# Kernel optimization log

Measured on AMD Instinct MI355X. Metric: run time of the kernel, lower is better.

The kernel has to match this reference:

```python
import jax, jax.numpy as jnp
import numpy as np
from jax import lax

DN = ('NCHW', 'OIHW', 'NCHW')


def conv3x3(x, w, b):
    return lax.conv_general_dilated(x, w, (1, 1), 'SAME', dimension_numbers=DN) + b[None, :, None, None]


def conv1x1(x, w, b):
    # w: [O, I] -> pointwise conv
    return jnp.einsum('oi,bihw->bohw', w, x) + b[None, :, None, None]


def sft(x0, x1, sc0w, sc0b, sc1w, sc1b, sh0w, sh0b, sh1w, sh1b):
    scale = conv1x1(jax.nn.leaky_relu(conv1x1(x1, sc0w, sc0b), 0.1), sc1w, sc1b)
    shift = conv1x1(jax.nn.leaky_relu(conv1x1(x1, sh0w, sh0b), 0.1), sh1w, sh1b)
    return x0 * (scale + 1.0) + shift


def deform_conv(x, offset, w, b):
    # torchvision DeformConv2d, 3x3, stride 1, pad 1, dilation 1, no mask.
    B, C, H, W = x.shape
    O = w.shape[0]
    K = 9
    off = offset.reshape(B, K, 2, H, W)  # (dy, dx) per kernel tap
    ki = jnp.arange(3, dtype=x.dtype) - 1.0
    ky = jnp.repeat(ki, 3)  # [9]
    kx = jnp.tile(ki, 3)
    hh = jnp.arange(H, dtype=x.dtype)
    ww = jnp.arange(W, dtype=x.dtype)
    py = off[:, :, 0] + hh[None, None, :, None] + ky[None, :, None, None]  # [B,K,H,W]
    px = off[:, :, 1] + ww[None, None, None, :] + kx[None, :, None, None]
    y0f = jnp.floor(py)
    x0f = jnp.floor(px)
    wy = (py - y0f)[:, None]  # [B,1,K,H,W]
    wx = (px - x0f)[:, None]
    y0 = y0f.astype(jnp.int32)
    x0i = x0f.astype(jnp.int32)
    x_flat = x.reshape(B, C, H * W)

    def gather(iy, ix):
        valid = (iy >= 0) & (iy < H) & (ix >= 0) & (ix < W)
        idx = (jnp.clip(iy, 0, H - 1) * W + jnp.clip(ix, 0, W - 1)).reshape(B, K * H * W)
        vals = jax.vmap(lambda xf, ii: xf[:, ii])(x_flat, idx)  # [B,C,K*H*W]
        return vals.reshape(B, C, K, H, W) * valid[:, None].astype(x.dtype)

    v00 = gather(y0, x0i)
    v01 = gather(y0, x0i + 1)
    v10 = gather(y0 + 1, x0i)
    v11 = gather(y0 + 1, x0i + 1)
    samp = (v00 * (1 - wy) * (1 - wx) + v01 * (1 - wy) * wx
            + v10 * wy * (1 - wx) + v11 * wy * wx)  # [B,C,K,H,W]
    return jnp.einsum('bckhw,ock->bohw', samp, w.reshape(O, C, K)) + b[None, :, None, None]


def setup_inputs() -> dict:
    key = jax.random.key(0)
    ks = jax.random.split(key, 32)
    B, C0, C1, H, W = 4, 128, 32, 96, 96
    f32 = jnp.float32
    d = {
        'x0': jax.random.normal(ks[0], (B, C0, H, W), f32),
        'x1': jax.random.normal(ks[1], (B, C1, H, W), f32),
        'w_off': jax.random.normal(ks[2], (18, C0, 3, 3), f32) * 0.02,
        'b_off': jnp.zeros((18,), f32),
        's1_sc0_w': jax.random.normal(ks[3], (C0, C1), f32) * 0.05,
        's1_sc0_b': jnp.zeros((C0,), f32),
        's1_sc1_w': jax.random.normal(ks[4], (C0, C0), f32) * 0.05,
        's1_sc1_b': jnp.zeros((C0,), f32),
        's1_sh0_w': jax.random.normal(ks[5], (C0, C1), f32) * 0.05,
        's1_sh0_b': jnp.zeros((C0,), f32),
        's1_sh1_w': jax.random.normal(ks[6], (C0, C0), f32) * 0.05,
        's1_sh1_b': jnp.zeros((C0,), f32),
        'w_d1': jax.random.normal(ks[7], (C0, C0, 3, 3), f32) * 0.03,
        'b_d1': jnp.zeros((C0,), f32),
        's2_sc0_w': jax.random.normal(ks[8], (C0, C1), f32) * 0.05,
        's2_sc0_b': jnp.zeros((C0,), f32),
        's2_sc1_w': jax.random.normal(ks[9], (C0, C0), f32) * 0.05,
        's2_sc1_b': jnp.zeros((C0,), f32),
        's2_sh0_w': jax.random.normal(ks[10], (C0, C1), f32) * 0.05,
        's2_sh0_b': jnp.zeros((C0,), f32),
        's2_sh1_w': jax.random.normal(ks[11], (C0, C0), f32) * 0.05,
        's2_sh1_b': jnp.zeros((C0,), f32),
        'w_d2': jax.random.normal(ks[12], (C0, C0, 3, 3), f32) * 0.03,
        'b_d2': jnp.zeros((C0,), f32),
    }
    return d


def reference(x0, x1, w_off, b_off,
              s1_sc0_w, s1_sc0_b, s1_sc1_w, s1_sc1_b,
              s1_sh0_w, s1_sh0_b, s1_sh1_w, s1_sh1_b,
              w_d1, b_d1,
              s2_sc0_w, s2_sc0_b, s2_sc1_w, s2_sc1_b,
              s2_sh0_w, s2_sh0_b, s2_sh1_w, s2_sh1_b,
              w_d2, b_d2):
    off = conv3x3(x0, w_off, b_off)
    fea = sft(x0, x1, s1_sc0_w, s1_sc0_b, s1_sc1_w, s1_sc1_b,
              s1_sh0_w, s1_sh0_b, s1_sh1_w, s1_sh1_b)
    fea = jax.nn.relu(deform_conv(fea, off, w_d1, b_d1))
    fea = sft(fea, x1, s2_sc0_w, s2_sc0_b, s2_sc1_w, s2_sc1_b,
              s2_sh0_w, s2_sh0_b, s2_sh1_w, s2_sh1_b)
    fea = deform_conv(fea, off, w_d2, b_d2)
    return x0 + fea
```

## Files before the change

### kernel.cpp

```cpp
#include <hip/hip_runtime.h>

typedef unsigned short u16;
typedef unsigned int   u32;
typedef __attribute__((ext_vector_type(8))) _Float16 f16x8;
typedef __attribute__((ext_vector_type(2))) float f32x2;
typedef __attribute__((ext_vector_type(4))) float f32x4;
typedef __attribute__((ext_vector_type(4))) unsigned int u32x4;

constexpr int B_  = 4;
constexpr int C0  = 128;
constexpr int C1  = 32;
constexpr int H_  = 96;
constexpr int W_  = 96;
constexpr int HW  = H_ * W_;
constexpr int PT  = 64;
constexpr int TPB = HW / PT;
constexpr int NTILE = B_ * TPB;

__device__ inline u16 f2h(float f) {
    _Float16 h = (_Float16)f;
    return __builtin_bit_cast(u16, h);
}

__global__ __launch_bounds__(256) void k_prep(
    const float* __restrict__ w_off,
    const float* __restrict__ wd1,  const float* __restrict__ wd2,
    const float* __restrict__ s1c0, const float* __restrict__ s1h0,
    const float* __restrict__ s2c0, const float* __restrict__ s2h0,
    const float* __restrict__ s1c1, const float* __restrict__ s1h1,
    const float* __restrict__ s2c1, const float* __restrict__ s2h1,
    float* __restrict__ wofft, u16* __restrict__ wdhi, u16* __restrict__ wdlo,
    u16* __restrict__ w0h,     u16* __restrict__ w1h)
{
    int t = blockIdx.x * 256 + threadIdx.x;
    if (t < C0 * 18 * 9) {
        int c = t / 162, r = t % 162, o = r / 9, tap = r % 9;
        wofft[t] = w_off[(o * C0 + c) * 9 + tap];
    }
    if (t < 2 * 9 * C0 * C0) {
        int d = t / (9 * C0 * C0), r = t % (9 * C0 * C0);
        int k = r / (C0 * C0), r2 = r % (C0 * C0), o = r2 / C0, c = r2 % C0;
        const float* wsrc = d ? wd2 : wd1;
        float wv = wsrc[(o * C0 + c) * 9 + k];
        _Float16 hi = (_Float16)wv;
        float rr = wv - (float)hi;
        wdhi[t] = __builtin_bit_cast(u16, hi);
        wdlo[t] = f2h(rr);
    }
    if (t < 4 * C0 * C1) {
        int m = t / (C0 * C1), i = t % (C0 * C1);
        const float* s = (m == 0) ? s1c0 : (m == 1) ? s1h0 : (m == 2) ? s2c0 : s2h0;
        w0h[t] = f2h(s[i]);
    }
    if (t < 4 * C0 * C0) {
        int m = t / (C0 * C0), i = t % (C0 * C0);
        const float* s = (m == 0) ? s1c1 : (m == 1) ? s1h1 : (m == 2) ? s2c1 : s2h1;
        w1h[t] = f2h(s[i]);
    }
}

__global__ __launch_bounds__(256) void k_conv_off(
    const float* __restrict__ x0, const float* __restrict__ wofft,
    const float* __restrict__ boff, float* __restrict__ off)
{
    int bx = blockIdx.x;
    int b  = bx / TPB;
    int p0 = (bx % TPB) * PT;
    int tid = threadIdx.x;
    int p   = tid & 63;
    int cq  = __builtin_amdgcn_readfirstlane(tid >> 6);
    int pos = p0 + p;
    int h = pos / W_, w = pos % W_;

    float acc[18];
#pragma unroll
    for (int o = 0; o < 18; ++o) acc[o] = 0.f;

    for (int cc = 0; cc < 32; ++cc) {
        int c = cq * 32 + cc;
        const float* xb = x0 + ((size_t)(b * C0 + c)) * HW;
        float v[9];
#pragma unroll
        for (int t = 0; t < 9; ++t) {
            int dy = t / 3 - 1, dx = t % 3 - 1;
            int hy = h + dy, wx = w + dx;
            bool ok = (hy >= 0) & (hy < H_) & (wx >= 0) & (wx < W_);
            v[t] = ok ? xb[hy * W_ + wx] : 0.f;
        }
        const float* wr = wofft + c * 162;
#pragma unroll
        for (int o = 0; o < 18; ++o)
#pragma unroll
            for (int t = 0; t < 9; ++t)
                acc[o] = fmaf(wr[o * 9 + t], v[t], acc[o]);
    }

    __shared__ float red[4][18][PT];
#pragma unroll
    for (int o = 0; o < 18; ++o) red[cq][o][p] = acc[o];
    __syncthreads();
    for (int idx = tid; idx < 18 * PT; idx += 256) {
        int o = idx / PT, pp = idx % PT;
        float s = red[0][o][pp] + red[1][o][pp] + red[2][o][pp] + red[3][o][pp]
                + boff[o];
        off[((size_t)(b * 18 + o)) * HW + p0 + pp] = s;
    }
}

template <int XSRC>
__global__ __launch_bounds__(512) void k_sft_mma(
    const float* __restrict__ xf,
    const float* __restrict__ xT,
    const float* __restrict__ x1,
    const u16* __restrict__ w0s, const u16* __restrict__ w0h,
    const u16* __restrict__ w1s, const u16* __restrict__ w1h,
    const float* __restrict__ b0s, const float* __restrict__ b0h,
    const float* __restrict__ b1s, const float* __restrict__ b1h,
    float* __restrict__ outT)
{
    __shared__ __align__(16) u16   x1t[64 * 32];
    __shared__ __align__(16) u16   hidt[2][64 * 128];
    __shared__ __align__(16) float outt[64 * 128];

    int bx = blockIdx.x, b = bx / TPB, p0 = (bx % TPB) * PT;
    int tid = threadIdx.x, l = tid & 63;
    int w = __builtin_amdgcn_readfirstlane(tid >> 6);
    f32x4 zz = {0.f, 0.f, 0.f, 0.f};

    for (int i = tid; i < C1 * PT; i += 512) {
        int ch = i >> 6, pos = i & 63;
        float v = x1[((size_t)(b * C1 + ch)) * HW + p0 + pos];
        x1t[pos * 32 + (ch ^ ((pos & 3) << 3))] = f2h(v);
    }
    __syncthreads();

    {
        int mt = w & 3, br = w >> 2;
        int pos = mt * 16 + (l & 15);
        int koff = (l >> 4) * 8;
        f16x8 a = *(const f16x8*)&x1t[pos * 32 + (koff ^ ((pos & 3) << 3))];
        const u16* w0 = br ? w0h : w0s;
        const float* bb = br ? b0h : b0s;
        u16* hrow = hidt[br];
#pragma unroll
        for (int nt = 0; nt < 8; ++nt) {
            int n = nt * 16 + (l & 15);
            f16x8 bfr = *(const f16x8*)&w0[n * 32 + koff];
            f32x4 h = __builtin_amdgcn_mfma_f32_16x16x32_f16(a, bfr, zz, 0, 0, 0);
            float bv = bb[n];
#pragma unroll
            for (int r = 0; r < 4; ++r) {
                float hv = h[r] + bv;
                hv = hv > 0.f ? hv : 0.1f * hv;
                int prow = mt * 16 + (l >> 4) * 4 + r;
                hrow[prow * 128 + (n ^ ((prow & 7) << 3))] = f2h(hv);
            }
        }
    }
    __syncthreads();

    f32x4 accS[4], accH[4];
#pragma unroll
    for (int nt = 0; nt < 4; ++nt) { accS[nt] = zz; accH[nt] = zz; }
    int mt = w & 3, nh = w >> 2;
    int pos = mt * 16 + (l & 15);
#pragma unroll
    for (int ks = 0; ks < 4; ++ks) {
        int kb = ks * 32 + (l >> 4) * 8;
        f16x8 aS = *(const f16x8*)&hidt[0][pos * 128 + (kb ^ ((pos & 7) << 3))];
        f16x8 aH = *(const f16x8*)&hidt[1][pos * 128 + (kb ^ ((pos & 7) << 3))];
#pragma unroll
        for (int nt = 0; nt < 4; ++nt) {
            int n = nh * 64 + nt * 16 + (l & 15);
            f16x8 bS = *(const f16x8*)&w1s[n * 128 + kb];
            f16x8 bH = *(const f16x8*)&w1h[n * 128 + kb];
            accS[nt] = __builtin_amdgcn_mfma_f32_16x16x32_f16(aS, bS, accS[nt], 0, 0, 0);
            accH[nt] = __builtin_amdgcn_mfma_f32_16x16x32_f16(aH, bH, accH[nt], 0, 0, 0);
        }
    }

#pragma unroll
    for (int nt = 0; nt < 4; ++nt) {
        int n = nh * 64 + nt * 16 + (l & 15);
        float scb = b1s[n], shb = b1h[n];
        float xv[4];
        if (XSRC == 0) {
            const float* xp = xf + ((size_t)(b * C0 + n)) * HW + p0 + mt * 16 + (l >> 4) * 4;
            f32x4 x4 = *(const f32x4*)xp;
#pragma unroll
            for (int r = 0; r < 4; ++r) xv[r] = x4[r];
        } else {
#pragma unroll
            for (int r = 0; r < 4; ++r)
                xv[r] = xT[((size_t)(b * HW + p0 + mt * 16 + (l >> 4) * 4 + r)) * C0 + n];
        }
#pragma unroll
        for (int r = 0; r < 4; ++r) {
            float scale = accS[nt][r] + scb + 1.f;
            float shift = accH[nt][r] + shb;
            outt[(mt * 16 + (l >> 4) * 4 + r) * 128 + n] = xv[r] * scale + shift;
        }
    }
    __syncthreads();

    float* dst = outT + ((size_t)(b * HW + p0)) * C0;
    for (int i = tid; i < 2048; i += 512)
        *(f32x4*)&dst[i * 4] = *(const f32x4*)&outt[i * 4];
}

template <int MODE>
__global__ __launch_bounds__(512, 4) void k_deform5(
    const float* __restrict__ srcT,
    const float* __restrict__ off,
    const u16* __restrict__ whi,
    const u16* __restrict__ wlo,
    const float* __restrict__ bias,
    const float* __restrict__ x0,
    float* __restrict__ outF,
    float* __restrict__ outT)
{
    constexpr int S = 136;
    __shared__ __align__(16) u16   smem[4 * 64 * S];
    __shared__ __align__(16) u16   cidx[9 * 64 * 4];
    __shared__ __align__(16) float cwt[9 * 64 * 2];
    u16* a_hi = smem;
    u16* a_lo = smem + 64 * S;
    u16* b_hi = smem + 2 * 64 * S;
    u16* b_lo = smem + 3 * 64 * S;

    int bx = blockIdx.x;
    bx = (bx & 7) * (NTILE / 8) + (bx >> 3);
    int b = bx / TPB, p0 = (bx % TPB) * PT;
    int tid = threadIdx.x, l = tid & 63;
    int w = __builtin_amdgcn_readfirstlane(tid >> 6);
    f32x4 zz = {0.f, 0.f, 0.f, 0.f};

    for (int e = tid; e < 9 * 64; e += 512) {
        int k = e >> 6, pp = e & 63;
        int pos = p0 + pp, h = pos / W_, wc = pos % W_;
        float dy = off[((size_t)(b * 18 + 2 * k)) * HW + pos];
        float dx = off[((size_t)(b * 18 + 2 * k + 1)) * HW + pos];
        float py = dy + (float)(h + k / 3 - 1);
        float px = dx + (float)(wc + k % 3 - 1);
        float yf = floorf(py), xf = floorf(px);
        int y0 = (int)yf, x0i = (int)xf;
        cwt[e * 2]     = py - yf;
        cwt[e * 2 + 1] = px - xf;
        int iy0 = min(max(y0, 0), H_ - 1),     iy1 = min(max(y0 + 1, 0), H_ - 1);
        int ix0 = min(max(x0i, 0), W_ - 1),    ix1 = min(max(x0i + 1, 0), W_ - 1);
        bool vy0 = (y0 >= 0) & (y0 < H_),      vy1 = (y0 + 1 >= 0) & (y0 + 1 < H_);
        bool vx0 = (x0i >= 0) & (x0i < W_),    vx1 = (x0i + 1 >= 0) & (x0i + 1 < W_);
        cidx[e * 4 + 0] = (u16)(iy0 * W_ + ix0) | ((vy0 & vx0) ? 0x8000 : 0);
        cidx[e * 4 + 1] = (u16)(iy0 * W_ + ix1) | ((vy0 & vx1) ? 0x8000 : 0);
        cidx[e * 4 + 2] = (u16)(iy1 * W_ + ix0) | ((vy1 & vx0) ? 0x8000 : 0);
        cidx[e * 4 + 3] = (u16)(iy1 * W_ + ix1) | ((vy1 & vx1) ? 0x8000 : 0);
    }
    __syncthreads();

    f32x4 acc[2][2];
#pragma unroll
    for (int hf = 0; hf < 2; ++hf)
#pragma unroll
        for (int nt = 0; nt < 2; ++nt) acc[hf][nt] = zz;

    int mt = w & 3, ng = w >> 2;
    int pos_r = mt * 16 + (l & 15);
    int so = tid >> 3, sp = tid & 7;
    const float* base  = srcT + (size_t)b * HW * C0;
    const float* lbase = base + 2 * l;

    f32x2 gv1[4][4], gv2[4][4];
    u32x4 rbh0, rbh1, rbl0, rbl1;

#define ISSUE_A(DST, KK, IOFF)                                                \
    {                                                                         \
        int ek = (KK) * 64 + w * 8 + (IOFF);                                  \
        _Pragma("unroll")                                                     \
        for (int i = 0; i < 4; ++i) {                                         \
            int e = ek + i;                                                   \
            u32 c01 = *(const u32*)&cidx[e * 4];                              \
            u32 c23 = *(const u32*)&cidx[e * 4 + 2];                          \
            DST[i][0] = *(const f32x2*)(lbase + (size_t)(c01 & 0x3fffu) * C0);\
            DST[i][1] = *(const f32x2*)(lbase + (size_t)((c01 >> 16) & 0x3fffu) * C0); \
            DST[i][2] = *(const f32x2*)(lbase + (size_t)(c23 & 0x3fffu) * C0);\
            DST[i][3] = *(const f32x2*)(lbase + (size_t)((c23 >> 16) & 0x3fffu) * C0); \
        }                                                                     \
    }

#define COMMIT_HALF(SRC, KK, IOFF)                                            \
    {                                                                         \
        int ek = (KK) * 64 + w * 8 + (IOFF);                                  \
        _Pragma("unroll")                                                     \
        for (int i = 0; i < 4; ++i) {                                         \
            int e = ek + i, pp = w * 8 + (IOFF) + i;                          \
            u32 c01 = *(const u32*)&cidx[e * 4];                              \
            u32 c23 = *(const u32*)&cidx[e * 4 + 2];                          \
            float wy = cwt[e * 2], wx = cwt[e * 2 + 1];                       \
            float aa  = wy * wx;                                              \
            float w11 = (c23 & 0x80000000u) ? aa : 0.f;                       \
            float w10 = (c23 & 0x8000u) ? (wy - aa) : 0.f;                    \
            float w01 = (c01 & 0x80000000u) ? (wx - aa) : 0.f;                \
            float w00 = (c01 & 0x8000u) ? (1.f - wy - wx + aa) : 0.f;         \
            float s0 = SRC[i][0][0] * w00 + SRC[i][1][0] * w01                \
                     + SRC[i][2][0] * w10 + SRC[i][3][0] * w11;               \
            float s1 = SRC[i][0][1] * w00 + SRC[i][1][1] * w01                \
                     + SRC[i][2][1] * w10 + SRC[i][3][1] * w11;               \
            _Float16 h0 = (_Float16)s0, h1 = (_Float16)s1;                    \
            float r0 = s0 - (float)h0, r1 = s1 - (float)h1;                   \
            u32 hv = (u32)__builtin_bit_cast(u16, h0)                         \
                   | ((u32)__builtin_bit_cast(u16, h1) << 16);                \
            u32 lv = (u32)f2h(r0) | ((u32)f2h(r1) << 16);                     \
            *(u32*)&a_hi[pp * S + 2 * l] = hv;                                \
            *(u32*)&a_lo[pp * S + 2 * l] = lv;                                \
        }                                                                     \
    }

#define ISSUE_B(KK, HF)                                                       \
    {                                                                         \
        int orow = (HF) * 64 + so;                                            \
        const u16* sh = whi + ((size_t)(KK) * C0 + orow) * C0 + sp * 16;      \
        const u16* sl = wlo + ((size_t)(KK) * C0 + orow) * C0 + sp * 16;      \
        rbh0 = *(const u32x4*)&sh[0];  rbh1 = *(const u32x4*)&sh[8];          \
        rbl0 = *(const u32x4*)&sl[0];  rbl1 = *(const u32x4*)&sl[8];          \
    }

#define WRITE_B()                                                             \
    {                                                                         \
        *(u32x4*)&b_hi[so * S + sp * 16]     = rbh0;                          \
        *(u32x4*)&b_hi[so * S + sp * 16 + 8] = rbh1;                          \
        *(u32x4*)&b_lo[so * S + sp * 16]     = rbl0;                          \
        *(u32x4*)&b_lo[so * S + sp * 16 + 8] = rbl1;                          \
    }

#define MFMA_HALF(HF)                                                         \
    {                                                                         \
        _Pragma("unroll")                                                     \
        for (int ks = 0; ks < 4; ++ks) {                                      \
            int kb = ks * 32 + (l >> 4) * 8;                                  \
            int ai = pos_r * S + kb;                                          \
            f16x8 ah = *(const f16x8*)&a_hi[ai];                              \
            f16x8 al = *(const f16x8*)&a_lo[ai];                              \
            _Pragma("unroll")                                                 \
            for (int nt = 0; nt < 2; ++nt) {                                  \
                int orow = ng * 32 + nt * 16 + (l & 15);                      \
                int bi = orow * S + kb;                                       \
                f16x8 bh = *(const f16x8*)&b_hi[bi];                          \
                f16x8 bl = *(const f16x8*)&b_lo[bi];                          \
                acc[HF][nt] = __builtin_amdgcn_mfma_f32_16x16x32_f16(ah, bh, acc[HF][nt], 0, 0, 0); \
                acc[HF][nt] = __builtin_amdgcn_mfma_f32_16x16x32_f16(al, bh, acc[HF][nt], 0, 0, 0); \
                acc[HF][nt] = __builtin_amdgcn_mfma_f32_16x16x32_f16(ah, bl, acc[HF][nt], 0, 0, 0); \
            }                                                                 \
        }                                                                     \
    }

    ISSUE_A(gv1, 0, 0)
    ISSUE_A(gv2, 0, 4)
    ISSUE_B(0, 0)

    for (int k = 0; k < 9; ++k) {
        COMMIT_HALF(gv1, k, 0)
        COMMIT_HALF(gv2, k, 4)
        WRITE_B()
        ISSUE_B(k, 1)
        if (k < 8) ISSUE_A(gv1, k + 1, 0)
        __builtin_amdgcn_sched_barrier(0);
        __syncthreads();
        MFMA_HALF(0)
        __syncthreads();
        WRITE_B()
        if (k < 8) { ISSUE_B(k + 1, 0) }
        if (k < 8) { ISSUE_A(gv2, k + 1, 4) }
        __builtin_amdgcn_sched_barrier(0);
        __syncthreads();
        MFMA_HALF(1)
        __syncthreads();
    }
#undef ISSUE_A
#undef COMMIT_HALF
#undef ISSUE_B
#undef WRITE_B
#undef MFMA_HALF

    if (MODE == 0) {
        float* otile = (float*)smem;
#pragma unroll
        for (int hf = 0; hf < 2; ++hf)
#pragma unroll
            for (int nt = 0; nt < 2; ++nt) {
                int o = hf * 64 + ng * 32 + nt * 16 + (l & 15);
                float bv = bias[o];
#pragma unroll
                for (int r = 0; r < 4; ++r) {
                    float v = acc[hf][nt][r] + bv;
                    v = v > 0.f ? v : 0.f;
                    otile[(mt * 16 + (l >> 4) * 4 + r) * 132 + o] = v;
                }
            }
        __syncthreads();
        float* dst = outT + ((size_t)(b * HW + p0)) * C0;
        for (int i = tid; i < 2048; i += 512) {
            int row = i >> 5, c = i & 31;
            *(f32x4*)&dst[row * 128 + c * 4] = *(const f32x4*)&otile[row * 132 + c * 4];
        }
    } else {
#pragma unroll
        for (int hf = 0; hf < 2; ++hf)
#pragma unroll
            for (int nt = 0; nt < 2; ++nt) {
                int o = hf * 64 + ng * 32 + nt * 16 + (l & 15);
                float bv = bias[o];
                size_t base_o = ((size_t)(b * C0 + o)) * HW + p0 + mt * 16 + (l >> 4) * 4;
                f32x4 x4 = *(const f32x4*)(x0 + base_o);
                f32x4 ov;
#pragma unroll
                for (int r = 0; r < 4; ++r) ov[r] = acc[hf][nt][r] + bv + x4[r];
                *(f32x4*)(outF + base_o) = ov;
            }
    }
}

constexpr size_t WB_OFF   = 0;
constexpr size_t WB_WOFFT = 2654208;
constexpr size_t WB_W0H   = 2737152;
constexpr size_t WB_W1H   = 2769920;
constexpr size_t WB_WDHI  = 2900992;
constexpr size_t WB_WDLO  = 4080640;
constexpr size_t WB_TA    = 5260288;
constexpr size_t WB_TB    = 24134656;

extern "C" void kernel_launch(void* const* d_in, const int* in_sizes, int n_in,
                              void* d_out, int out_size, void* d_ws, size_t ws_size,
                              hipStream_t stream)
{
    const float* x0      = (const float*)d_in[0];
    const float* x1      = (const float*)d_in[1];
    const float* w_off   = (const float*)d_in[2];
    const float* b_off   = (const float*)d_in[3];
    const float* s1_sc0w = (const float*)d_in[4];
    const float* s1_sc0b = (const float*)d_in[5];
    const float* s1_sc1w = (const float*)d_in[6];
    const float* s1_sc1b = (const float*)d_in[7];
    const float* s1_sh0w = (const float*)d_in[8];
    const float* s1_sh0b = (const float*)d_in[9];
    const float* s1_sh1w = (const float*)d_in[10];
    const float* s1_sh1b = (const float*)d_in[11];
    const float* w_d1    = (const float*)d_in[12];
    const float* b_d1    = (const float*)d_in[13];
    const float* s2_sc0w = (const float*)d_in[14];
    const float* s2_sc0b = (const float*)d_in[15];
    const float* s2_sc1w = (const float*)d_in[16];
    const float* s2_sc1b = (const float*)d_in[17];
    const float* s2_sh0w = (const float*)d_in[18];
    const float* s2_sh0b = (const float*)d_in[19];
    const float* s2_sh1w = (const float*)d_in[20];
    const float* s2_sh1b = (const float*)d_in[21];
    const float* w_d2    = (const float*)d_in[22];
    const float* b_d2    = (const float*)d_in[23];

    char* wsb = (char*)d_ws;
    float* off   = (float*)(wsb + WB_OFF);
    float* wofft = (float*)(wsb + WB_WOFFT);
    u16*   w0h   = (u16*)(wsb + WB_W0H);
    u16*   w1h   = (u16*)(wsb + WB_W1H);
    u16*   wdhi  = (u16*)(wsb + WB_WDHI);
    u16*   wdlo  = (u16*)(wsb + WB_WDLO);
    float* TA    = (float*)(wsb + WB_TA);
    float* TB    = (float*)(wsb + WB_TB);

    k_prep<<<1152, 256, 0, stream>>>(w_off, w_d1, w_d2,
                                     s1_sc0w, s1_sh0w, s2_sc0w, s2_sh0w,
                                     s1_sc1w, s1_sh1w, s2_sc1w, s2_sh1w,
                                     wofft, wdhi, wdlo, w0h, w1h);
    k_conv_off<<<NTILE, 256, 0, stream>>>(x0, wofft, b_off, off);
    k_sft_mma<0><<<NTILE, 512, 0, stream>>>(x0, nullptr, x1,
                                            w0h, w0h + 4096,
                                            w1h, w1h + 16384,
                                            s1_sc0b, s1_sh0b, s1_sc1b, s1_sh1b, TA);
    k_deform5<0><<<NTILE, 512, 0, stream>>>(TA, off, wdhi, wdlo, b_d1,
                                            nullptr, nullptr, TB);
    k_sft_mma<1><<<NTILE, 512, 0, stream>>>(nullptr, TB, x1,
                                            w0h + 8192, w0h + 12288,
                                            w1h + 32768, w1h + 49152,
                                            s2_sc0b, s2_sh0b, s2_sc1b, s2_sh1b, TA);
    k_deform5<1><<<NTILE, 512, 0, stream>>>(TA, off, wdhi + 9 * 16384, wdlo + 9 * 16384,
                                            b_d2, x0, (float*)d_out, nullptr);
}
```

Baseline: 365.2 us.

## Restructure deform conv to 32x32 MFMA with K-halved weight staging

The deformable conv kernel now has each wave compute a 32x32 output tile with 32x32x16 f16 MFMAs instead of four 16x16 tiles. Weights are staged in 64-wide K halves, with full __syncthreads replaced by lgkmcnt waits plus s_barrier, and setprio raised around the MFMA phases. The SFT kernel drops its shared-memory output tile and writes its transposed output directly to global memory with a 6-block occupancy hint. The larger MFMA tile is meant to cut LDS traffic per flop. In exchange, the SFT stores become strided and less coalesced, and the lighter barrier scheme is harder to keep correct.

Measured after the change: 376.8 us. 1.03x slower.

```diff
diff --git a/kernel.cpp b/kernel.cpp
--- a/kernel.cpp
+++ b/kernel.cpp
@@ -5,6 +5,7 @@
 typedef __attribute__((ext_vector_type(8))) _Float16 f16x8;
 typedef __attribute__((ext_vector_type(2))) float f32x2;
 typedef __attribute__((ext_vector_type(4))) float f32x4;
+typedef __attribute__((ext_vector_type(16))) float f32x16;
 typedef __attribute__((ext_vector_type(4))) unsigned int u32x4;
 
 constexpr int B_  = 4;
@@ -108,7 +109,7 @@
 }
 
 template <int XSRC>
-__global__ __launch_bounds__(512) void k_sft_mma(
+__global__ __launch_bounds__(512, 6) void k_sft_mma(
     const float* __restrict__ xf,
     const float* __restrict__ xT,
     const float* __restrict__ x1,
@@ -118,9 +119,8 @@
     const float* __restrict__ b1s, const float* __restrict__ b1h,
     float* __restrict__ outT)
 {
-    __shared__ __align__(16) u16   x1t[64 * 32];
-    __shared__ __align__(16) u16   hidt[2][64 * 128];
-    __shared__ __align__(16) float outt[64 * 128];
+    __shared__ __align__(16) u16 x1t[64 * 32];
+    __shared__ __align__(16) u16 hidt[2][64 * 128];
 
     int bx = blockIdx.x, b = bx / TPB, p0 = (bx % TPB) * PT;
     int tid = threadIdx.x, l = tid & 63;
@@ -198,18 +198,14 @@
         for (int r = 0; r < 4; ++r) {
             float scale = accS[nt][r] + scb + 1.f;
             float shift = accH[nt][r] + shb;
-            outt[(mt * 16 + (l >> 4) * 4 + r) * 128 + n] = xv[r] * scale + shift;
-        }
-    }
-    __syncthreads();
-
-    float* dst = outT + ((size_t)(b * HW + p0)) * C0;
-    for (int i = tid; i < 2048; i += 512)
-        *(f32x4*)&dst[i * 4] = *(const f32x4*)&outt[i * 4];
+            outT[((size_t)(b * HW + p0 + mt * 16 + (l >> 4) * 4 + r)) * C0 + n]
+                = xv[r] * scale + shift;
+        }
+    }
 }
 
 template <int MODE>
-__global__ __launch_bounds__(512, 4) void k_deform5(
+__global__ __launch_bounds__(512, 4) void k_deform10(
     const float* __restrict__ srcT,
     const float* __restrict__ off,
     const u16* __restrict__ whi,
@@ -219,21 +215,20 @@
     float* __restrict__ outF,
     float* __restrict__ outT)
 {
-    constexpr int S = 136;
-    __shared__ __align__(16) u16   smem[4 * 64 * S];
+    constexpr int SA = 136;
+    constexpr int SB = 72;
+    __shared__ __align__(16) u16   a_buf[2][64 * SA];
+    __shared__ __align__(16) u16   b_buf[2][128 * SB];
     __shared__ __align__(16) u16   cidx[9 * 64 * 4];
     __shared__ __align__(16) float cwt[9 * 64 * 2];
-    u16* a_hi = smem;
-    u16* a_lo = smem + 64 * S;
-    u16* b_hi = smem + 2 * 64 * S;
-    u16* b_lo = smem + 3 * 64 * S;
 
     int bx = blockIdx.x;
     bx = (bx & 7) * (NTILE / 8) + (bx >> 3);
     int b = bx / TPB, p0 = (bx % TPB) * PT;
     int tid = threadIdx.x, l = tid & 63;
     int w = __builtin_amdgcn_readfirstlane(tid >> 6);
-    f32x4 zz = {0.f, 0.f, 0.f, 0.f};
+    int mh = w & 1, ng = w >> 1;
+    int lr = l & 31, ksel = l >> 5;
 
     for (int e = tid; e < 9 * 64; e += 512) {
         int k = e >> 6, pp = e & 63;
@@ -257,22 +252,17 @@
     }
     __syncthreads();
 
-    f32x4 acc[2][2];
-#pragma unroll
-    for (int hf = 0; hf < 2; ++hf)
-#pragma unroll
-        for (int nt = 0; nt < 2; ++nt) acc[hf][nt] = zz;
-
-    int mt = w & 3, ng = w >> 2;
-    int pos_r = mt * 16 + (l & 15);
-    int so = tid >> 3, sp = tid & 7;
-    const float* base  = srcT + (size_t)b * HW * C0;
-    const float* lbase = base + 2 * l;
+    f32x16 acc;
+#pragma unroll
+    for (int i = 0; i < 16; ++i) acc[i] = 0.f;
+
+    const float* lbase = srcT + (size_t)b * HW * C0 + 2 * l;
+    int wrow = tid >> 2, wseg = tid & 3;
 
     f32x2 gv1[4][4], gv2[4][4];
-    u32x4 rbh0, rbh1, rbl0, rbl1;
-
-#define ISSUE_A(DST, KK, IOFF)                                                \
+    u32x4 wbh[2], wbl[2];
+
+#define ISSUE_G(DST, KK, IOFF)                                                \
     {                                                                         \
         int ek = (KK) * 64 + w * 8 + (IOFF);                                  \
         _Pragma("unroll")                                                     \
@@ -287,7 +277,7 @@
         }                                                                     \
     }
 
-#define COMMIT_HALF(SRC, KK, IOFF)                                            \
+#define COMMIT_CH(SRC, KK, IOFF)                                              \
     {                                                                         \
         int ek = (KK) * 64 + w * 8 + (IOFF);                                  \
         _Pragma("unroll")                                                     \
@@ -310,92 +300,103 @@
             u32 hv = (u32)__builtin_bit_cast(u16, h0)                         \
                    | ((u32)__builtin_bit_cast(u16, h1) << 16);                \
             u32 lv = (u32)f2h(r0) | ((u32)f2h(r1) << 16);                     \
-            *(u32*)&a_hi[pp * S + 2 * l] = hv;                                \
-            *(u32*)&a_lo[pp * S + 2 * l] = lv;                                \
+            *(u32*)&a_buf[0][pp * SA + 2 * l] = hv;                           \
+            *(u32*)&a_buf[1][pp * SA + 2 * l] = lv;                           \
         }                                                                     \
     }
 
-#define ISSUE_B(KK, HF)                                                       \
+#define ISSUE_W(KK, KH)                                                       \
     {                                                                         \
-        int orow = (HF) * 64 + so;                                            \
-        const u16* sh = whi + ((size_t)(KK) * C0 + orow) * C0 + sp * 16;      \
-        const u16* sl = wlo + ((size_t)(KK) * C0 + orow) * C0 + sp * 16;      \
-        rbh0 = *(const u32x4*)&sh[0];  rbh1 = *(const u32x4*)&sh[8];          \
-        rbl0 = *(const u32x4*)&sl[0];  rbl1 = *(const u32x4*)&sl[8];          \
+        const u16* sh = whi + (size_t)(KK) * 16384 + wrow * 128 + (KH) * 64 + wseg * 16; \
+        const u16* sl = wlo + (size_t)(KK) * 16384 + wrow * 128 + (KH) * 64 + wseg * 16; \
+        wbh[0] = *(const u32x4*)&sh[0];  wbh[1] = *(const u32x4*)&sh[8];      \
+        wbl[0] = *(const u32x4*)&sl[0];  wbl[1] = *(const u32x4*)&sl[8];      \
     }
 
 #define WRITE_B()                                                             \
     {                                                                         \
-        *(u32x4*)&b_hi[so * S + sp * 16]     = rbh0;                          \
-        *(u32x4*)&b_hi[so * S + sp * 16 + 8] = rbh1;                          \
-        *(u32x4*)&b_lo[so * S + sp * 16]     = rbl0;                          \
-        *(u32x4*)&b_lo[so * S + sp * 16 + 8] = rbl1;                          \
-    }
-
-#define MFMA_HALF(HF)                                                         \
+        *(u32x4*)&b_buf[0][wrow * SB + wseg * 16]     = wbh[0];               \
+        *(u32x4*)&b_buf[0][wrow * SB + wseg * 16 + 8] = wbh[1];               \
+        *(u32x4*)&b_buf[1][wrow * SB + wseg * 16]     = wbl[0];               \
+        *(u32x4*)&b_buf[1][wrow * SB + wseg * 16 + 8] = wbl[1];               \
+    }
+
+#define MFMA_PH(KH)                                                           \
     {                                                                         \
         _Pragma("unroll")                                                     \
         for (int ks = 0; ks < 4; ++ks) {                                      \
-            int kb = ks * 32 + (l >> 4) * 8;                                  \
-            int ai = pos_r * S + kb;                                          \
-            f16x8 ah = *(const f16x8*)&a_hi[ai];                              \
-            f16x8 al = *(const f16x8*)&a_lo[ai];                              \
-            _Pragma("unroll")                                                 \
-            for (int nt = 0; nt < 2; ++nt) {                                  \
-                int orow = ng * 32 + nt * 16 + (l & 15);                      \
-                int bi = orow * S + kb;                                       \
-                f16x8 bh = *(const f16x8*)&b_hi[bi];                          \
-                f16x8 bl = *(const f16x8*)&b_lo[bi];                          \
-                acc[HF][nt] = __builtin_amdgcn_mfma_f32_16x16x32_f16(ah, bh, acc[HF][nt], 0, 0, 0); \
-                acc[HF][nt] = __builtin_amdgcn_mfma_f32_16x16x32_f16(al, bh, acc[HF][nt], 0, 0, 0); \
-                acc[HF][nt] = __builtin_amdgcn_mfma_f32_16x16x32_f16(ah, bl, acc[HF][nt], 0, 0, 0); \
-            }                                                                 \
+            int kA = (KH) * 64 + ks * 16 + ksel * 8;                          \
+            int kB = ks * 16 + ksel * 8;                                      \
+            f16x8 ah = *(const f16x8*)&a_buf[0][(mh * 32 + lr) * SA + kA];    \
+            f16x8 al = *(const f16x8*)&a_buf[1][(mh * 32 + lr) * SA + kA];    \
+            f16x8 bh = *(const f16x8*)&b_buf[0][(ng * 32 + lr) * SB + kB];    \
+            f16x8 bl = *(const f16x8*)&b_buf[1][(ng * 32 + lr) * SB + kB];    \
+            acc = __builtin_amdgcn_mfma_f32_32x32x16_f16(ah, bh, acc, 0, 0, 0); \
+            acc = __builtin_amdgcn_mfma_f32_32x32x16_f16(al, bh, acc, 0, 0, 0); \
+            acc = __builtin_amdgcn_mfma_f32_32x32x16_f16(ah, bl, acc, 0, 0, 0); \
         }                                                                     \
     }
 
-    ISSUE_A(gv1, 0, 0)
-    ISSUE_A(gv2, 0, 4)
-    ISSUE_B(0, 0)
+#define LGKM_BAR                                                              \
+    asm volatile("s_waitcnt lgkmcnt(0)" ::: "memory");                        \
+    __builtin_amdgcn_s_barrier();
+
+    ISSUE_G(gv1, 0, 0)
+    ISSUE_G(gv2, 0, 4)
+    ISSUE_W(0, 0)
+    COMMIT_CH(gv1, 0, 0)
+    COMMIT_CH(gv2, 0, 4)
+    WRITE_B()
+    ISSUE_W(0, 1)
+    __builtin_amdgcn_sched_barrier(0);
+    LGKM_BAR
 
     for (int k = 0; k < 9; ++k) {
-        COMMIT_HALF(gv1, k, 0)
-        COMMIT_HALF(gv2, k, 4)
+        __builtin_amdgcn_s_setprio(1);
+        MFMA_PH(0)
+        __builtin_amdgcn_s_setprio(0);
+        if (k < 8) ISSUE_G(gv1, k + 1, 0)
+        __builtin_amdgcn_sched_barrier(0);
+        LGKM_BAR
         WRITE_B()
-        ISSUE_B(k, 1)
-        if (k < 8) ISSUE_A(gv1, k + 1, 0)
+        if (k < 8) { ISSUE_W(k + 1, 0) ISSUE_G(gv2, k + 1, 4) }
         __builtin_amdgcn_sched_barrier(0);
+        LGKM_BAR
+        __builtin_amdgcn_s_setprio(1);
+        MFMA_PH(1)
+        __builtin_amdgcn_s_setprio(0);
+        LGKM_BAR
+        if (k < 8) {
+            COMMIT_CH(gv1, k + 1, 0)
+            COMMIT_CH(gv2, k + 1, 4)
+            WRITE_B()
+            ISSUE_W(k + 1, 1)
+        }
+        __builtin_amdgcn_sched_barrier(0);
+        LGKM_BAR
+    }
+#undef ISSUE_G
+#undef COMMIT_CH
+#undef ISSUE_W
+#undef WRITE_B
+#undef MFMA_PH
+#undef LGKM_BAR
+
+    int o = ng * 32 + lr;
+    float bv = bias[o];
+    if (MODE == 0) {
         __syncthreads();
-        MFMA_HALF(0)
-        __syncthreads();
-        WRITE_B()
-        if (k < 8) { ISSUE_B(k + 1, 0) }
-        if (k < 8) { ISSUE_A(gv2, k + 1, 4) }
-        __builtin_amdgcn_sched_barrier(0);
-        __syncthreads();
-        MFMA_HALF(1)
-        __syncthreads();
-    }
-#undef ISSUE_A
-#undef COMMIT_HALF
-#undef ISSUE_B
-#undef WRITE_B
-#undef MFMA_HALF
-
-    if (MODE == 0) {
-        float* otile = (float*)smem;
-#pragma unroll
-        for (int hf = 0; hf < 2; ++hf)
-#pragma unroll
-            for (int nt = 0; nt < 2; ++nt) {
-                int o = hf * 64 + ng * 32 + nt * 16 + (l & 15);
-                float bv = bias[o];
-#pragma unroll
-                for (int r = 0; r < 4; ++r) {
-                    float v = acc[hf][nt][r] + bv;
-                    v = v > 0.f ? v : 0.f;
-                    otile[(mt * 16 + (l >> 4) * 4 + r) * 132 + o] = v;
-                }
+        float* otile = (float*)&a_buf[0][0];
+#pragma unroll
+        for (int q = 0; q < 4; ++q) {
+            int pr = mh * 32 + q * 8 + 4 * ksel;
+#pragma unroll
+            for (int r = 0; r < 4; ++r) {
+                float v = acc[q * 4 + r] + bv;
+                v = v > 0.f ? v : 0.f;
+                otile[(pr + r) * 132 + o] = v;
             }
+        }
         __syncthreads();
         float* dst = outT + ((size_t)(b * HW + p0)) * C0;
         for (int i = tid; i < 2048; i += 512) {
@@ -404,18 +405,15 @@
         }
     } else {
 #pragma unroll
-        for (int hf = 0; hf < 2; ++hf)
-#pragma unroll
-            for (int nt = 0; nt < 2; ++nt) {
-                int o = hf * 64 + ng * 32 + nt * 16 + (l & 15);
-                float bv = bias[o];
-                size_t base_o = ((size_t)(b * C0 + o)) * HW + p0 + mt * 16 + (l >> 4) * 4;
-                f32x4 x4 = *(const f32x4*)(x0 + base_o);
-                f32x4 ov;
-#pragma unroll
-                for (int r = 0; r < 4; ++r) ov[r] = acc[hf][nt][r] + bv + x4[r];
-                *(f32x4*)(outF + base_o) = ov;
-            }
+        for (int q = 0; q < 4; ++q) {
+            int pr = mh * 32 + q * 8 + 4 * ksel;
+            size_t base_o = ((size_t)(b * C0 + o)) * HW + p0 + pr;
+            f32x4 x4 = *(const f32x4*)(x0 + base_o);
+            f32x4 ov;
+#pragma unroll
+            for (int r = 0; r < 4; ++r) ov[r] = acc[q * 4 + r] + bv + x4[r];
+            *(f32x4*)(outF + base_o) = ov;
+        }
     }
 }
 
@@ -476,12 +474,12 @@
                                             w0h, w0h + 4096,
                                             w1h, w1h + 16384,
                                             s1_sc0b, s1_sh0b, s1_sc1b, s1_sh1b, TA);
-    k_deform5<0><<<NTILE, 512, 0, stream>>>(TA, off, wdhi, wdlo, b_d1,
-                                            nullptr, nullptr, TB);
+    k_deform10<0><<<NTILE, 512, 0, stream>>>(TA, off, wdhi, wdlo, b_d1,
+                                             nullptr, nullptr, TB);
     k_sft_mma<1><<<NTILE, 512, 0, stream>>>(nullptr, TB, x1,
                                             w0h + 8192, w0h + 12288,
                                             w1h + 32768, w1h + 49152,
                                             s2_sc0b, s2_sh0b, s2_sc1b, s2_sh1b, TA);
-    k_deform5<1><<<NTILE, 512, 0, stream>>>(TA, off, wdhi + 9 * 16384, wdlo + 9 * 16384,
-                                            b_d2, x0, (float*)d_out, nullptr);
-}
+    k_deform10<1><<<NTILE, 512, 0, stream>>>(TA, off, wdhi + 9 * 16384, wdlo + 9 * 16384,
+                                             b_d2, x0, (float*)d_out, nullptr);
+}
```
